# Kernel optimization log

Hardware: AMD Instinct MI355X
Metric: run time of the kernel (lower is better)

The kernel has to match this reference:

```python
import jax, jax.numpy as jnp
import numpy as np

LEAKY_SLOPE = 0.05        # self.alpha is overwritten to 0.05 in __init__
NEG_INF = -9.0e15         # masking constant from the source
THRESH = 0.5              # connection_threshold

B, N, F = 8, 2048, 128


def setup_inputs() -> dict:
    key = jax.random.key(0)
    k1, k2, k3, k4, k5 = jax.random.split(key, 5)
    h = jax.random.normal(k1, (B, N, F), dtype=jnp.float32)
    W = jax.random.normal(k2, (F, F), dtype=jnp.float32) * (1.414 / np.sqrt(F))
    a = jax.random.normal(k3, (2 * F, 1), dtype=jnp.float32) * 0.1
    A1 = jax.random.normal(k4, (4 * N, N), dtype=jnp.float32) * (1.414 / np.sqrt(N))
    A2 = jax.random.normal(k5, (N, 4 * N), dtype=jnp.float32) * (1.414 / np.sqrt(4 * N))
    return {"h": h, "W": W, "a": a, "A1": A1, "A2": A2}


def reference(h, W, a, A1, A2):
    f = W.shape[0]
    # Wh = h @ W^T  (torch Linear stores weight as [out, in])
    Wh = jnp.einsum('bnf,gf->bng', h, W)                       # [B,N,F]
    # additive GAT scores: e[b,i,j] = leaky_relu(Wh_i.a1 + Wh_j.a2)
    Wh1 = Wh @ a[:f, :]                                        # [B,N,1]
    Wh2 = Wh @ a[f:, :]                                        # [B,N,1]
    e = Wh1 + jnp.swapaxes(Wh2, 1, 2)                          # [B,N,N]
    e = jnp.where(e > 0, e, LEAKY_SLOPE * e)                   # LeakyReLU(0.05)
    # learned adjacency gate over last dim (computed in the original forward
    # but never used for the returned output -> dead code; kept for fidelity)
    hid = jax.nn.sigmoid(jnp.einsum('bij,hj->bih', e, A1))     # [B,N,4N]
    adj = jax.nn.sigmoid(e + jnp.einsum('bih,jh->bij', hid, A2))
    adj = jnp.where(adj > THRESH, adj, 0.0)                    # unused downstream
    # masked softmax attention over e itself
    attention = jax.nn.softmax(jnp.where(e > 0, e, NEG_INF), axis=2)
    # dropout is identity in eval mode (training=False)
    h_prime = jnp.einsum('bij,bjf->bif', attention, Wh)        # [B,N,F]
    return jax.nn.elu(h_prime)                                 # concat=True branch
```

## Files before the change

kernel.cpp:

```cpp
#include <hip/hip_runtime.h>
#include <math.h>

#define BB 8
#define NN 2048
#define FF 128
#define CH 128
#define CHSZ 16

__global__ __launch_bounds__(512) void k1_wh(
        const float* __restrict__ h, const float* __restrict__ W,
        const float* __restrict__ a, float* __restrict__ Wh,
        float* __restrict__ s1, float* __restrict__ s2) {
    __shared__ __align__(16) float Wt[64][132];
    __shared__ float hs[64][65];
    const int tid = threadIdx.x;
    const int row0 = blockIdx.x * 64;
    const int gq = tid & 15;
    const int rq = tid >> 4;

    float acc[2][8];
#pragma unroll
    for (int r = 0; r < 2; ++r)
#pragma unroll
        for (int g = 0; g < 8; ++g) acc[r][g] = 0.f;

    for (int half = 0; half < 2; ++half) {
        __syncthreads();
        for (int idx = tid; idx < 64 * 128; idx += 512) {
            int g = idx >> 6, fl = idx & 63;
            Wt[fl][g] = W[g * 128 + half * 64 + fl];
        }
        for (int idx = tid; idx < 64 * 64; idx += 512) {
            int r = idx >> 6, fl = idx & 63;
            hs[r][fl] = h[(row0 + r) * 128 + half * 64 + fl];
        }
        __syncthreads();
        for (int fl = 0; fl < 64; ++fl) {
            float4 w0 = *(const float4*)&Wt[fl][gq * 8];
            float4 w1 = *(const float4*)&Wt[fl][gq * 8 + 4];
            float h0 = hs[rq * 2 + 0][fl];
            float h1 = hs[rq * 2 + 1][fl];
            acc[0][0] += h0 * w0.x; acc[0][1] += h0 * w0.y;
            acc[0][2] += h0 * w0.z; acc[0][3] += h0 * w0.w;
            acc[0][4] += h0 * w1.x; acc[0][5] += h0 * w1.y;
            acc[0][6] += h0 * w1.z; acc[0][7] += h0 * w1.w;
            acc[1][0] += h1 * w0.x; acc[1][1] += h1 * w0.y;
            acc[1][2] += h1 * w0.z; acc[1][3] += h1 * w0.w;
            acc[1][4] += h1 * w1.x; acc[1][5] += h1 * w1.y;
            acc[1][6] += h1 * w1.z; acc[1][7] += h1 * w1.w;
        }
    }

    float a1v[8], a2v[8];
#pragma unroll
    for (int g = 0; g < 8; ++g) {
        a1v[g] = a[gq * 8 + g];
        a2v[g] = a[128 + gq * 8 + g];
    }
#pragma unroll
    for (int r = 0; r < 2; ++r) {
        int row = row0 + rq * 2 + r;
        *(float4*)&Wh[row * 128 + gq * 8] =
            make_float4(acc[r][0], acc[r][1], acc[r][2], acc[r][3]);
        *(float4*)&Wh[row * 128 + gq * 8 + 4] =
            make_float4(acc[r][4], acc[r][5], acc[r][6], acc[r][7]);
        float p1 = 0.f, p2 = 0.f;
#pragma unroll
        for (int g = 0; g < 8; ++g) {
            p1 += acc[r][g] * a1v[g];
            p2 += acc[r][g] * a2v[g];
        }
#pragma unroll
        for (int s = 1; s < 16; s <<= 1) {
            p1 += __shfl_xor(p1, s, 64);
            p2 += __shfl_xor(p2, s, 64);
        }
        if (gq == 0) { s1[row] = p1; s2[row] = p2; }
    }
}

__global__ __launch_bounds__(1024) void k2_sort(
        const float* __restrict__ s2, float* __restrict__ s2s,
        int* __restrict__ idxs, float* __restrict__ ps,
        float* __restrict__ sufexp) {
    __shared__ float sk[2048];
    __shared__ int   si[2048];
    __shared__ float scanA[1024];
    const int t = threadIdx.x;
    const int b = blockIdx.x;
    const int base = b * NN;

    sk[t] = s2[base + t];            si[t] = t;
    sk[t + 1024] = s2[base + t + 1024]; si[t + 1024] = t + 1024;

    for (int k = 2; k <= 2048; k <<= 1) {
        for (int j = k >> 1; j > 0; j >>= 1) {
            __syncthreads();
            int i = ((t & ~(j - 1)) << 1) | (t & (j - 1));
            int l = i | j;
            float va = sk[i], vb = sk[l];
            bool asc = ((i & k) == 0);
            bool sw = asc ? (va > vb) : (va < vb);
            if (sw) {
                int ia = si[i], ib = si[l];
                sk[i] = vb; sk[l] = va;
                si[i] = ib; si[l] = ia;
            }
        }
    }
    __syncthreads();
    float M = sk[2047];
    float p0 = expf(sk[2 * t] - M);
    float p1 = expf(sk[2 * t + 1] - M);
    scanA[t] = p0 + p1;
    __syncthreads();
    for (int s = 1; s < 1024; s <<= 1) {
        float add = (t + s < 1024) ? scanA[t + s] : 0.f;
        __syncthreads();
        scanA[t] += add;
        __syncthreads();
    }
    float excl = (t < 1023) ? scanA[t + 1] : 0.f;
    s2s[base + 2 * t] = sk[2 * t];
    s2s[base + 2 * t + 1] = sk[2 * t + 1];
    idxs[base + 2 * t] = si[2 * t];
    idxs[base + 2 * t + 1] = si[2 * t + 1];
    ps[base + 2 * t] = p0;
    ps[base + 2 * t + 1] = p1;
    sufexp[base + 2 * t] = excl + p1 + p0;
    sufexp[base + 2 * t + 1] = excl + p1;
}

__global__ __launch_bounds__(128) void k3_scan(
        const float* __restrict__ Wh, const float* __restrict__ s2s,
        const int* __restrict__ idxs, const float* __restrict__ ps,
        float* __restrict__ partial, float* __restrict__ chunktot,
        float* __restrict__ chunku) {
    const int blk = blockIdx.x;
    const int b = blk / CH, c = blk % CH;
    const int base = b * NN;
    const int f = threadIdx.x;
    float acc = 0.f, accu = 0.f;
#pragma unroll
    for (int tt = CHSZ - 1; tt >= 0; --tt) {
        int r = c * CHSZ + tt;
        int j = idxs[base + r];
        float pv = ps[base + r];
        float w = Wh[(base + j) * 128 + f];
        acc += pv * w;
        accu += w;
        partial[(base + r) * 128 + f] = acc;
    }
    chunktot[(b * CH + c) * 128 + f] = acc;
    chunku[(b * CH + c) * 128 + f] = accu;
    (void)s2s;
}

__global__ __launch_bounds__(128) void k3b_chunksuf(
        const float* __restrict__ chunktot, const float* __restrict__ chunku,
        float* __restrict__ chunksuf, float* __restrict__ meanv) {
    const int b = blockIdx.x;
    const int f = threadIdx.x;
    float acc = 0.f, tu = 0.f;
    for (int c = CH - 1; c >= 0; --c) {
        chunksuf[(b * CH + c) * 128 + f] = acc;
        acc += chunktot[(b * CH + c) * 128 + f];
        tu += chunku[(b * CH + c) * 128 + f];
    }
    meanv[b * 128 + f] = tu * (1.f / (float)NN);
}

__global__ __launch_bounds__(256) void k4_out(
        const float* __restrict__ s1, const float* __restrict__ s2s,
        const float* __restrict__ sufexp, const float* __restrict__ partial,
        const float* __restrict__ chunksuf, const float* __restrict__ meanv,
        float* __restrict__ out) {
    const int tid = threadIdx.x;
    const int rowg = blockIdx.x * 2 + (tid >> 7);
    const int f = tid & 127;
    const int b = rowg >> 11;
    const int base = b * NN;
    const float s1v = s1[rowg];
    int lo = 0, hi = NN;
    while (lo < hi) {
        int mid = (lo + hi) >> 1;
        if (s1v + s2s[base + mid] > 0.f) hi = mid; else lo = mid + 1;
    }
    float v;
    if (lo == NN) {
        v = meanv[b * 128 + f];
    } else {
        int c = lo >> 4;
        float num = partial[(base + lo) * 128 + f] +
                    chunksuf[(b * CH + c) * 128 + f];
        v = num / sufexp[base + lo];
    }
    out[rowg * 128 + f] = (v > 0.f) ? v : expm1f(v);
}

extern "C" void kernel_launch(void* const* d_in, const int* in_sizes, int n_in,
                              void* d_out, int out_size, void* d_ws, size_t ws_size,
                              hipStream_t stream) {
    (void)in_sizes; (void)n_in; (void)out_size; (void)ws_size;
    const float* h = (const float*)d_in[0];
    const float* W = (const float*)d_in[1];
    const float* a = (const float*)d_in[2];
    float* out = (float*)d_out;

    float* Wh      = (float*)d_ws;
    float* partial = Wh + 2097152;
    float* s1      = partial + 2097152;
    float* s2      = s1 + 16384;
    float* s2s     = s2 + 16384;
    float* sufexp  = s2s + 16384;
    float* ps      = sufexp + 16384;
    int*   idxs    = (int*)(ps + 16384);
    float* chunktot = (float*)(idxs + 16384);
    float* chunku   = chunktot + 131072;
    float* chunksuf = chunku + 131072;
    float* meanv    = chunksuf + 131072;

    k1_wh<<<BB * NN / 64, 512, 0, stream>>>(h, W, a, Wh, s1, s2);
    k2_sort<<<BB, 1024, 0, stream>>>(s2, s2s, idxs, ps, sufexp);
    k3_scan<<<BB * CH, 128, 0, stream>>>(Wh, s2s, idxs, ps, partial, chunktot, chunku);
    k3b_chunksuf<<<BB, 128, 0, stream>>>(chunktot, chunku, chunksuf, meanv);
    k4_out<<<BB * NN / 2, 256, 0, stream>>>(s1, s2s, sufexp, partial, chunksuf, meanv, out);
}
```

Before: 201.7 us.

## Replace single-block bitonic sort with parallel rank sort and fold exp-scan into chunk scan

Swaps the per-batch 1024-thread bitonic sort, which has many barrier-separated stages on only 8 blocks, for a counting rank sort spread over 64 blocks. Each thread compares its value against all 2048 entries in shared memory and scatters to its rank. The exponent weights and their suffix sums are no longer computed in the sort kernel: they are recomputed inside the chunk scan and combined through a new per-chunk suffix array. This trades O(N log^2 N) synchronised work for O(N^2) barrier-free compares spread across more of the GPU.

Result: slower. 255.9 us (+26.9%).

```diff
diff --git a/kernel.cpp b/kernel.cpp
--- a/kernel.cpp
+++ b/kernel.cpp
@@ -79,102 +79,80 @@
     }
 }
 
-__global__ __launch_bounds__(1024) void k2_sort(
+__global__ __launch_bounds__(256) void k2_rank(
         const float* __restrict__ s2, float* __restrict__ s2s,
-        int* __restrict__ idxs, float* __restrict__ ps,
-        float* __restrict__ sufexp) {
-    __shared__ float sk[2048];
-    __shared__ int   si[2048];
-    __shared__ float scanA[1024];
+        int* __restrict__ idxs) {
+    __shared__ float ls[NN];
     const int t = threadIdx.x;
-    const int b = blockIdx.x;
+    const int b = blockIdx.x >> 3;
+    const int seg = blockIdx.x & 7;
     const int base = b * NN;
-
-    sk[t] = s2[base + t];            si[t] = t;
-    sk[t + 1024] = s2[base + t + 1024]; si[t + 1024] = t + 1024;
-
-    for (int k = 2; k <= 2048; k <<= 1) {
-        for (int j = k >> 1; j > 0; j >>= 1) {
-            __syncthreads();
-            int i = ((t & ~(j - 1)) << 1) | (t & (j - 1));
-            int l = i | j;
-            float va = sk[i], vb = sk[l];
-            bool asc = ((i & k) == 0);
-            bool sw = asc ? (va > vb) : (va < vb);
-            if (sw) {
-                int ia = si[i], ib = si[l];
-                sk[i] = vb; sk[l] = va;
-                si[i] = ib; si[l] = ia;
-            }
-        }
-    }
+    for (int i = t; i < NN; i += 256) ls[i] = s2[base + i];
     __syncthreads();
-    float M = sk[2047];
-    float p0 = expf(sk[2 * t] - M);
-    float p1 = expf(sk[2 * t + 1] - M);
-    scanA[t] = p0 + p1;
-    __syncthreads();
-    for (int s = 1; s < 1024; s <<= 1) {
-        float add = (t + s < 1024) ? scanA[t + s] : 0.f;
-        __syncthreads();
-        scanA[t] += add;
-        __syncthreads();
-    }
-    float excl = (t < 1023) ? scanA[t + 1] : 0.f;
-    s2s[base + 2 * t] = sk[2 * t];
-    s2s[base + 2 * t + 1] = sk[2 * t + 1];
-    idxs[base + 2 * t] = si[2 * t];
-    idxs[base + 2 * t + 1] = si[2 * t + 1];
-    ps[base + 2 * t] = p0;
-    ps[base + 2 * t + 1] = p1;
-    sufexp[base + 2 * t] = excl + p1 + p0;
-    sufexp[base + 2 * t + 1] = excl + p1;
+    const int j = seg * 256 + t;
+    const float v = ls[j];
+    int rank = 0;
+#pragma unroll 8
+    for (int k = 0; k < NN; ++k) {
+        float vk = ls[k];
+        rank += (vk < v) | ((vk == v) & (k < j));
+    }
+    s2s[base + rank] = v;
+    idxs[base + rank] = j;
 }
 
 __global__ __launch_bounds__(128) void k3_scan(
         const float* __restrict__ Wh, const float* __restrict__ s2s,
-        const int* __restrict__ idxs, const float* __restrict__ ps,
-        float* __restrict__ partial, float* __restrict__ chunktot,
-        float* __restrict__ chunku) {
+        const int* __restrict__ idxs,
+        float* __restrict__ partial, float* __restrict__ psuf,
+        float* __restrict__ chunktot, float* __restrict__ chunku,
+        float* __restrict__ chunkp) {
     const int blk = blockIdx.x;
-    const int b = blk / CH, c = blk % CH;
+    const int b = blk >> 7, c = blk & 127;
     const int base = b * NN;
     const int f = threadIdx.x;
-    float acc = 0.f, accu = 0.f;
+    const float M = s2s[base + NN - 1];
+    float acc = 0.f, accu = 0.f, pacc = 0.f;
 #pragma unroll
     for (int tt = CHSZ - 1; tt >= 0; --tt) {
         int r = c * CHSZ + tt;
-        int j = idxs[base + r];
-        float pv = ps[base + r];
-        float w = Wh[(base + j) * 128 + f];
+        int jj = idxs[base + r];
+        float pv = expf(s2s[base + r] - M);
+        float w = Wh[(base + jj) * 128 + f];
         acc += pv * w;
         accu += w;
+        pacc += pv;
         partial[(base + r) * 128 + f] = acc;
+        if (f == 0) psuf[base + r] = pacc;
     }
     chunktot[(b * CH + c) * 128 + f] = acc;
     chunku[(b * CH + c) * 128 + f] = accu;
-    (void)s2s;
+    if (f == 0) chunkp[b * CH + c] = pacc;
 }
 
 __global__ __launch_bounds__(128) void k3b_chunksuf(
         const float* __restrict__ chunktot, const float* __restrict__ chunku,
-        float* __restrict__ chunksuf, float* __restrict__ meanv) {
+        const float* __restrict__ chunkp,
+        float* __restrict__ chunksuf, float* __restrict__ chunkpsuf,
+        float* __restrict__ meanv) {
     const int b = blockIdx.x;
     const int f = threadIdx.x;
-    float acc = 0.f, tu = 0.f;
+    float acc = 0.f, tu = 0.f, pacc = 0.f;
     for (int c = CH - 1; c >= 0; --c) {
         chunksuf[(b * CH + c) * 128 + f] = acc;
         acc += chunktot[(b * CH + c) * 128 + f];
         tu += chunku[(b * CH + c) * 128 + f];
+        if (f == 0) chunkpsuf[b * CH + c] = pacc;
+        pacc += chunkp[b * CH + c];
     }
     meanv[b * 128 + f] = tu * (1.f / (float)NN);
 }
 
 __global__ __launch_bounds__(256) void k4_out(
         const float* __restrict__ s1, const float* __restrict__ s2s,
-        const float* __restrict__ sufexp, const float* __restrict__ partial,
-        const float* __restrict__ chunksuf, const float* __restrict__ meanv,
-        float* __restrict__ out) {
+        const float* __restrict__ psuf, const float* __restrict__ chunkpsuf,
+        const float* __restrict__ partial, const float* __restrict__ chunksuf,
+        const float* __restrict__ meanv, float* __restrict__ out) {
     const int tid = threadIdx.x;
     const int rowg = blockIdx.x * 2 + (tid >> 7);
     const int f = tid & 127;
@@ -193,7 +171,8 @@
         int c = lo >> 4;
         float num = partial[(base + lo) * 128 + f] +
                     chunksuf[(b * CH + c) * 128 + f];
-        v = num / sufexp[base + lo];
+        float den = psuf[base + lo] + chunkpsuf[b * CH + c];
+        v = num / den;
     }
     out[rowg * 128 + f] = (v > 0.f) ? v : expm1f(v);
 }
@@ -207,22 +186,26 @@
     const float* a = (const float*)d_in[2];
     float* out = (float*)d_out;
 
-    float* Wh      = (float*)d_ws;
-    float* partial = Wh + 2097152;
-    float* s1      = partial + 2097152;
-    float* s2      = s1 + 16384;
-    float* s2s     = s2 + 16384;
-    float* sufexp  = s2s + 16384;
-    float* ps      = sufexp + 16384;
-    int*   idxs    = (int*)(ps + 16384);
+    float* Wh       = (float*)d_ws;
+    float* partial  = Wh + 2097152;
+    float* s1       = partial + 2097152;
+    float* s2       = s1 + 16384;
+    float* s2s      = s2 + 16384;
+    float* psuf     = s2s + 16384;
+    int*   idxs     = (int*)(psuf + 16384);
     float* chunktot = (float*)(idxs + 16384);
     float* chunku   = chunktot + 131072;
     float* chunksuf = chunku + 131072;
-    float* meanv    = chunksuf + 131072;
+    float* chunkp   = chunksuf + 131072;
+    float* chunkpsuf= chunkp + 1024;
+    float* meanv    = chunkpsuf + 1024;
 
     k1_wh<<<BB * NN / 64, 512, 0, stream>>>(h, W, a, Wh, s1, s2);
-    k2_sort<<<BB, 1024, 0, stream>>>(s2, s2s, idxs, ps, sufexp);
-    k3_scan<<<BB * CH, 128, 0, stream>>>(Wh, s2s, idxs, ps, partial, chunktot, chunku);
-    k3b_chunksuf<<<BB, 128, 0, stream>>>(chunktot, chunku, chunksuf, meanv);
-    k4_out<<<BB * NN / 2, 256, 0, stream>>>(s1, s2s, sufexp, partial, chunksuf, meanv, out);
-}
+    k2_rank<<<BB * 8, 256, 0, stream>>>(s2, s2s, idxs);
+    k3_scan<<<BB * CH, 128, 0, stream>>>(Wh, s2s, idxs, partial, psuf,
+                                         chunktot, chunku, chunkp);
+    k3b_chunksuf<<<BB, 128, 0, stream>>>(chunktot, chunku, chunkp,
+                                         chunksuf, chunkpsuf, meanv);
+    k4_out<<<BB * NN / 2, 256, 0, stream>>>(s1, s2s, psuf, chunkpsuf,
+                                            partial, chunksuf, meanv, out);
+}
```
